# Kernel optimization log

Hardware: AMD Instinct MI355X
Metric: run time of the kernel (lower is better)

## Reference

```python
import jax, jax.numpy as jnp
import numpy as np

B, N, IN = 4, 1024, 768
H, F = 8, 96
ALPHA = 0.2
NEG = -1e30  # stands in for -inf in masked_fill; exp underflows to 0 identically


def setup_inputs() -> dict:
    key = jax.random.key(0)
    k1, k2, k3, k4 = jax.random.split(key, 4)
    node_features = jax.random.normal(k1, (B, N, IN), dtype=jnp.float32)
    attention_mask = jax.random.randint(k2, (B, N), 0, 2, dtype=jnp.int32)
    # torch Linear(in, H*F, bias=False): y = x @ W  (W stored here as [in, H*F])
    W = jax.random.normal(k3, (IN, H * F), dtype=jnp.float32) * (1.0 / np.sqrt(IN))
    # torch Linear(2*F, 1, bias=False): a-vector of length 2*F, shared across heads
    a = jax.random.normal(k4, (2 * F,), dtype=jnp.float32) * (1.0 / np.sqrt(2 * F))
    return {"node_features": node_features, "attention_mask": attention_mask, "W": W, "a": a}


def reference(node_features, attention_mask, W, a):
    b, n, _ = node_features.shape
    Wh = (node_features @ W).reshape(b, n, H, F)          # [B,N,H,F]
    a1, a2 = a[:F], a[F:]                                  # split additive attention vector
    # a([Wh_i ; Wh_j]) = Wh_i.a1 + Wh_j.a2  -> broadcast-add, no (B,N,N,H,2F) concat
    f1 = jnp.einsum('bnhf,f->bhn', Wh, a1)                 # query half [B,H,N]
    f2 = jnp.einsum('bnhf,f->bhn', Wh, a2)                 # key half   [B,H,N]
    e = f1[:, :, :, None] + f2[:, :, None, :]              # [B,H,N,N] (i=query, j=key)
    e = jnp.where(e >= 0, e, ALPHA * e)                    # leaky_relu
    mask = (attention_mask == 0)[:, None, None, :]         # mask keys j
    e = jnp.where(mask, NEG, e)
    attn = jax.nn.softmax(e, axis=-1)                      # [B,H,N,N]
    h = jnp.einsum('bhij,bjhf->bihf', attn, Wh)            # [B,N,H,F]
    return h.reshape(b, n, H * F)                          # concat=True
```

## Files before the change

kernel.cpp:

```cpp
#include <hip/hip_runtime.h>
#include <hip/hip_bf16.h>

#define ALPHA 0.2f
#define LOG2E 1.44269504f

#define VB_OFFB 0
#define XB_OFFB 6291456
#define WB_OFFB (XB_OFFB + 6291456)
#define F1P_OFFB (WB_OFFB + 1179648)
#define F2P_OFFB (F1P_OFFB + 786432)

typedef __attribute__((ext_vector_type(8))) unsigned short us8;
typedef __attribute__((ext_vector_type(8))) short s8;
typedef __attribute__((ext_vector_type(4))) float f32x4;
typedef __attribute__((ext_vector_type(4))) unsigned int u32x4;

__device__ inline unsigned short f2bf(float x) {
    __hip_bfloat16 h = __float2bfloat16(x);
    return reinterpret_cast<unsigned short&>(h);
}

__device__ __forceinline__ void gload16(const void* g, void* lds) {
    __builtin_amdgcn_global_load_lds((const unsigned int*)g, (unsigned int*)lds,
                                     16, 0, 0);
}

__global__ __launch_bounds__(256) void prep_all(const float* __restrict__ X,
                                                const float* __restrict__ W,
                                                unsigned short* __restrict__ Xb,
                                                unsigned short* __restrict__ Wb) {
    if (blockIdx.x < 1536) {
        const int i = (blockIdx.x * 256 + threadIdx.x) * 8;
        float4 v0 = *(const float4*)&X[i];
        float4 v1 = *(const float4*)&X[i + 4];
        ushort4 p0, p1;
        p0.x = f2bf(v0.x); p0.y = f2bf(v0.y); p0.z = f2bf(v0.z); p0.w = f2bf(v0.w);
        p1.x = f2bf(v1.x); p1.y = f2bf(v1.y); p1.z = f2bf(v1.z); p1.w = f2bf(v1.w);
        *(ushort4*)&Xb[i] = p0;
        *(ushort4*)&Xb[i + 4] = p1;
    } else {
        const int id = (blockIdx.x - 1536) * 256 + threadIdx.x;
        const int l = id & 63;
        const int ks = (id >> 6) & 1;
        const int cg4 = (id >> 7) & 3;
        const int kc = id >> 9;
        const int kt = kc / 12;
        const int ct = kc - kt * 12;
        const int k0 = kt * 64 + ks * 32 + (l >> 4) * 8;
        const int n = ct * 64 + cg4 * 16 + (l & 15);
        ushort4 p0, p1;
        p0.x = f2bf(W[(size_t)(k0 + 0) * 768 + n]);
        p0.y = f2bf(W[(size_t)(k0 + 1) * 768 + n]);
        p0.z = f2bf(W[(size_t)(k0 + 2) * 768 + n]);
        p0.w = f2bf(W[(size_t)(k0 + 3) * 768 + n]);
        p1.x = f2bf(W[(size_t)(k0 + 4) * 768 + n]);
        p1.y = f2bf(W[(size_t)(k0 + 5) * 768 + n]);
        p1.z = f2bf(W[(size_t)(k0 + 6) * 768 + n]);
        p1.w = f2bf(W[(size_t)(k0 + 7) * 768 + n]);
        *(ushort4*)&Wb[(size_t)id * 8 + 0] = p0;
        *(ushort4*)&Wb[(size_t)id * 8 + 4] = p1;
    }
}

__global__ __launch_bounds__(256) void gemm_s(const unsigned short* __restrict__ Xb,
                                              const unsigned short* __restrict__ Wb,
                                              const float* __restrict__ a,
                                              unsigned short* __restrict__ Vb,
                                              float* __restrict__ f1p,
                                              float* __restrict__ f2p) {
    __shared__ __align__(16) unsigned short Xs[2][4096];
    __shared__ __align__(16) unsigned short Ws[2][4096];

    const int tid = threadIdx.x;
    const int l = tid & 63;
    const int w = tid >> 6;
    const int wr = w >> 1, wc = w & 1;
    const int nid = (blockIdx.x & 7) * 96 + (blockIdx.x >> 3);
    const int bx = nid % 12;
    const int row0 = (nid / 12) * 64;

    const int xrow_base = w * 16 + (l >> 3);
    const int xkb_log8 = ((l & 7) ^ (l >> 3)) * 8;

    f32x4 acc[2][2];
#pragma unroll
    for (int i = 0; i < 2; ++i)
#pragma unroll
        for (int j = 0; j < 2; ++j) acc[i][j] = (f32x4){0.f, 0.f, 0.f, 0.f};

#pragma unroll
    for (int q = 0; q < 2; ++q) {
        const int g16 = w * 2 + q;
        gload16(Xb + (size_t)(row0 + xrow_base + q * 8) * 768 + xkb_log8,
                &Xs[0][g16 * 512]);
        gload16(Wb + (size_t)(0 * 12 + bx) * 4096 + g16 * 512 + l * 8,
                &Ws[0][g16 * 512]);
    }

    int buf = 0;
    for (int kt = 0; kt < 12; ++kt) {
        __syncthreads();
        if (kt < 11) {
            const int k0n = (kt + 1) * 64;
#pragma unroll
            for (int q = 0; q < 2; ++q) {
                const int g16 = w * 2 + q;
                gload16(Xb + (size_t)(row0 + xrow_base + q * 8) * 768 + k0n + xkb_log8,
                        &Xs[buf ^ 1][g16 * 512]);
                gload16(Wb + (size_t)((kt + 1) * 12 + bx) * 4096 + g16 * 512 + l * 8,
                        &Ws[buf ^ 1][g16 * 512]);
            }
        }
#pragma unroll
        for (int ks = 0; ks < 2; ++ks) {
            s8 af[2], bfr[2];
#pragma unroll
            for (int fr = 0; fr < 2; ++fr) {
                const int row = wr * 32 + fr * 16 + (l & 15);
                const int slot = (ks * 4 + (l >> 4)) ^ (row & 7);
                af[fr] = *(const s8*)((const char*)&Xs[buf][0] + row * 128 + slot * 16);
            }
#pragma unroll
            for (int cg = 0; cg < 2; ++cg) {
                bfr[cg] = *(const s8*)((const char*)&Ws[buf][0] +
                                       (((wc * 2 + cg) * 2 + ks) * 64 + l) * 16);
            }
#pragma unroll
            for (int fr = 0; fr < 2; ++fr)
#pragma unroll
                for (int cg = 0; cg < 2; ++cg)
                    acc[fr][cg] = __builtin_amdgcn_mfma_f32_16x16x32_bf16(
                        af[fr], bfr[cg], acc[fr][cg], 0, 0, 0);
        }
        buf ^= 1;
    }

#pragma unroll
    for (int fr = 0; fr < 2; ++fr) {
#pragma unroll
        for (int cg = 0; cg < 2; ++cg) {
            const int jglob = row0 + wr * 32 + fr * 16 + (l >> 4) * 4;
            const int b = jglob >> 10;
            const int jn = jglob & 1023;
            const int jc = jn >> 7;
            const int ks4 = (jn >> 5) & 3;
            const int kg = (jn >> 3) & 3;
            const int e0 = jn & 7;
            const int g0 = bx * 64 + wc * 32 + cg * 16;
            const int h = g0 / 96;
            const int ft = (g0 - h * 96) >> 4;
            const int fc = l & 15;
            const size_t ibase =
                (((((size_t)(b * 8 + h) * 8 + jc) * 4 + ks4) * 4 + kg) * 6 + ft) * 128 +
                fc * 8 + e0;
            ushort4 pk;
            pk.x = f2bf(acc[fr][cg][0]);
            pk.y = f2bf(acc[fr][cg][1]);
            pk.z = f2bf(acc[fr][cg][2]);
            pk.w = f2bf(acc[fr][cg][3]);
            *(ushort4*)&Vb[ibase] = pk;
        }
    }

#pragma unroll
    for (int cg = 0; cg < 2; ++cg) {
        const int c = bx * 64 + wc * 32 + cg * 16 + (l & 15);
        const int h = c / 96;
        const int f = c - h * 96;
        const float av1 = a[f];
        const float av2 = a[96 + f];
        const int g = bx * 4 + wc * 2 + cg;
#pragma unroll
        for (int fr = 0; fr < 2; ++fr) {
            const int jglob = row0 + wr * 32 + fr * 16 + (l >> 4) * 4;
#pragma unroll
            for (int r = 0; r < 4; ++r) {
                float s1 = acc[fr][cg][r] * av1;
                float s2 = acc[fr][cg][r] * av2;
#pragma unroll
                for (int m = 1; m < 16; m <<= 1) {
                    s1 += __shfl_xor(s1, m);
                    s2 += __shfl_xor(s2, m);
                }
                if ((l & 15) == 0) {
                    f1p[(size_t)(jglob + r) * 48 + g] = s1;
                    f2p[(size_t)(jglob + r) * 48 + g] = s2;
                }
            }
        }
    }
}

__global__ __launch_bounds__(256) void attn_fast(const unsigned short* __restrict__ Vb,
                                                 const float* __restrict__ f1p,
                                                 const float* __restrict__ f2p,
                                                 const int* __restrict__ mask,
                                                 float* __restrict__ out) {
    __shared__ __align__(16) unsigned short Vs[2][12288];
    __shared__ float g2_s[1024];

    const int tid = threadIdx.x;
    const int lane = tid & 63;
    const int w = tid >> 6;
    const int kg = lane >> 4;
    const int fcr = lane & 15;
    const int nid = (blockIdx.x & 7) * 64 + (blockIdx.x >> 3);
    const int it = nid & 15;
    const int bh = nid >> 4;
    const int b = bh >> 3;
    const int h = bh & 7;

    const size_t vbase = (size_t)bh * 98304;

    for (int j = tid; j < 1024; j += 256) {
        const float* p2 = f2p + (size_t)(b * 1024 + j) * 48 + h * 6;
        float s = ((p2[0] + p2[1]) + (p2[2] + p2[3])) + (p2[4] + p2[5]);
        g2_s[j] = (mask[b * 1024 + j] != 0) ? s * LOG2E : -20000.f;
    }
    const float* p1 = f1p + (size_t)(b * 1024 + it * 64 + w * 16 + fcr) * 48 + h * 6;
    const float f1v = (((p1[0] + p1[1]) + (p1[2] + p1[3])) + (p1[4] + p1[5])) * LOG2E;

#pragma unroll
    for (int r = 0; r < 6; ++r) {
        const int s = r * 256 + tid;
        gload16(Vb + vbase + (size_t)s * 8, &Vs[0][s * 8]);
    }

    f32x4 acc[6];
#pragma unroll
    for (int ft = 0; ft < 6; ++ft) acc[ft] = (f32x4){0.f, 0.f, 0.f, 0.f};
    float ls = 0.f;

    int buf = 0;
    for (int c = 0; c < 8; ++c) {
        __syncthreads();
        if (c < 7) {
#pragma unroll
            for (int r = 0; r < 6; ++r) {
                const int s = r * 256 + tid;
                gload16(Vb + vbase + (size_t)(c + 1) * 12288 + (size_t)s * 8,
                        &Vs[buf ^ 1][s * 8]);
            }
        }
        const unsigned short* vsb = &Vs[buf][0];
#pragma unroll
        for (int ks = 0; ks < 4; ++ks) {
            const int jb = c * 128 + ks * 32 + kg * 8;
            float4 ga = *(const float4*)&g2_s[jb];
            float4 gb = *(const float4*)&g2_s[jb + 4];
            float g[8] = {ga.x, ga.y, ga.z, ga.w, gb.x, gb.y, gb.z, gb.w};
            u32x4 afu;
#pragma unroll
            for (int ep = 0; ep < 4; ++ep) {
                float t0 = f1v + g[2 * ep];
                float t1 = f1v + g[2 * ep + 1];
                float l0 = fmaxf(t0, ALPHA * t0);
                float l1 = fmaxf(t1, ALPHA * t1);
                float p0 = exp2f(l0);
                float p1 = exp2f(l1);
                ls += p0 + p1;
                unsigned int pk;
                asm("v_cvt_pk_bf16_f32 %0, %1, %2" : "=v"(pk) : "v"(p0), "v"(p1));
                afu[ep] = pk;
            }
            s8 af = __builtin_bit_cast(s8, afu);
            const unsigned short* vp = vsb + ((ks * 4 + kg) * 6) * 128 + fcr * 8;
#pragma unroll
            for (int ft = 0; ft < 6; ++ft) {
                us8 bvu = *(const us8*)(vp + ft * 128);
                acc[ft] = __builtin_amdgcn_mfma_f32_16x16x32_bf16(
                    af, (s8)bvu, acc[ft], 0, 0, 0);
            }
        }
        buf ^= 1;
    }

    ls += __shfl_xor(ls, 16);
    ls += __shfl_xor(ls, 32);
    float inv[4];
#pragma unroll
    for (int r = 0; r < 4; ++r) inv[r] = 1.0f / __shfl(ls, kg * 4 + r);

    const int irow0 = it * 64 + w * 16 + kg * 4;
#pragma unroll
    for (int r = 0; r < 4; ++r) {
        const size_t ob = (size_t)(b * 1024 + irow0 + r) * 768 + h * 96 + fcr;
#pragma unroll
        for (int ft = 0; ft < 6; ++ft) {
            out[ob + ft * 16] = acc[ft][r] * inv[r];
        }
    }
}

extern "C" void kernel_launch(void* const* d_in, const int* in_sizes, int n_in,
                              void* d_out, int out_size, void* d_ws, size_t ws_size,
                              hipStream_t stream) {
    const float* X = (const float*)d_in[0];
    const int* mask = (const int*)d_in[1];
    const float* W = (const float*)d_in[2];
    const float* a = (const float*)d_in[3];
    float* out = (float*)d_out;
    char* ws = (char*)d_ws;

    unsigned short* Vb = (unsigned short*)(ws + VB_OFFB);
    unsigned short* Xb = (unsigned short*)(ws + XB_OFFB);
    unsigned short* Wb = (unsigned short*)(ws + WB_OFFB);
    float* f1p = (float*)(ws + F1P_OFFB);
    float* f2p = (float*)(ws + F2P_OFFB);

    prep_all<<<1824, 256, 0, stream>>>(X, W, Xb, Wb);
    gemm_s<<<768, 256, 0, stream>>>(Xb, Wb, a, Vb, f1p, f2p);
    attn_fast<<<512, 256, 0, stream>>>(Vb, f1p, f2p, mask, out);
}
```

Baseline: 50.45 us.

## Pre-swizzle X into MFMA fragment layout and load GEMM operands directly to registers

The prep kernel now writes X in bf16 directly in the per-lane MFMA A-fragment order (16-row tiles by 32-k slots), matching the existing pre-packed W layout. The GEMM then drops LDS staging and barriers entirely, loading each wave's fragments straight from global memory into registers with a register double buffer. This removes LDS traffic and __syncthreads. In exchange, operands that were shared between waves in a block are now re-read from global/L2 by each wave, and the prep kernel's X reads become strided rather than contiguous.

```diff
diff --git a/kernel.cpp b/kernel.cpp
--- a/kernel.cpp
+++ b/kernel.cpp
@@ -5,8 +5,8 @@
 #define LOG2E 1.44269504f
 
 #define VB_OFFB 0
-#define XB_OFFB 6291456
-#define WB_OFFB (XB_OFFB + 6291456)
+#define XF_OFFB 6291456
+#define WB_OFFB (XF_OFFB + 6291456)
 #define F1P_OFFB (WB_OFFB + 1179648)
 #define F2P_OFFB (F1P_OFFB + 786432)
 
@@ -27,17 +27,24 @@
 
 __global__ __launch_bounds__(256) void prep_all(const float* __restrict__ X,
                                                 const float* __restrict__ W,
-                                                unsigned short* __restrict__ Xb,
+                                                unsigned short* __restrict__ Xf,
                                                 unsigned short* __restrict__ Wb) {
     if (blockIdx.x < 1536) {
-        const int i = (blockIdx.x * 256 + threadIdx.x) * 8;
-        float4 v0 = *(const float4*)&X[i];
-        float4 v1 = *(const float4*)&X[i + 4];
+        const int f = blockIdx.x * 256 + threadIdx.x;
+        const int l = f & 63;
+        const int t = f >> 6;
+        const int kslot = t % 24;
+        const int rt = t / 24;
+        const int row = rt * 16 + (l & 15);
+        const int k0 = kslot * 32 + (l >> 4) * 8;
+        const float* xp = X + (size_t)row * 768 + k0;
+        float4 v0 = *(const float4*)xp;
+        float4 v1 = *(const float4*)(xp + 4);
         ushort4 p0, p1;
         p0.x = f2bf(v0.x); p0.y = f2bf(v0.y); p0.z = f2bf(v0.z); p0.w = f2bf(v0.w);
         p1.x = f2bf(v1.x); p1.y = f2bf(v1.y); p1.z = f2bf(v1.z); p1.w = f2bf(v1.w);
-        *(ushort4*)&Xb[i] = p0;
-        *(ushort4*)&Xb[i + 4] = p1;
+        *(ushort4*)&Xf[(size_t)f * 8 + 0] = p0;
+        *(ushort4*)&Xf[(size_t)f * 8 + 4] = p1;
     } else {
         const int id = (blockIdx.x - 1536) * 256 + threadIdx.x;
         const int l = id & 63;
@@ -62,15 +69,12 @@
     }
 }
 
-__global__ __launch_bounds__(256) void gemm_s(const unsigned short* __restrict__ Xb,
-                                              const unsigned short* __restrict__ Wb,
+__global__ __launch_bounds__(256) void gemm_r(const unsigned short* __restrict__ Xf_,
+                                              const unsigned short* __restrict__ Wb_,
                                               const float* __restrict__ a,
                                               unsigned short* __restrict__ Vb,
                                               float* __restrict__ f1p,
                                               float* __restrict__ f2p) {
-    __shared__ __align__(16) unsigned short Xs[2][4096];
-    __shared__ __align__(16) unsigned short Ws[2][4096];
-
     const int tid = threadIdx.x;
     const int l = tid & 63;
     const int w = tid >> 6;
@@ -78,9 +82,14 @@
     const int nid = (blockIdx.x & 7) * 96 + (blockIdx.x >> 3);
     const int bx = nid % 12;
     const int row0 = (nid / 12) * 64;
-
-    const int xrow_base = w * 16 + (l >> 3);
-    const int xkb_log8 = ((l & 7) ^ (l >> 3)) * 8;
+    const int rt0 = (nid / 12) * 4;
+
+    const us8* Xf = (const us8*)Xf_;
+    const us8* Wf = (const us8*)Wb_;
+
+    const us8* xb0 = Xf + ((size_t)(rt0 + wr * 2 + 0) * 24) * 64 + l;
+    const us8* xb1 = Xf + ((size_t)(rt0 + wr * 2 + 1) * 24) * 64 + l;
+    const us8* wb0 = Wf + (size_t)bx * 512 + (size_t)(wc * 2) * 128 + l;
 
     f32x4 acc[2][2];
 #pragma unroll
@@ -88,51 +97,39 @@
 #pragma unroll
         for (int j = 0; j < 2; ++j) acc[i][j] = (f32x4){0.f, 0.f, 0.f, 0.f};
 
-#pragma unroll
-    for (int q = 0; q < 2; ++q) {
-        const int g16 = w * 2 + q;
-        gload16(Xb + (size_t)(row0 + xrow_base + q * 8) * 768 + xkb_log8,
-                &Xs[0][g16 * 512]);
-        gload16(Wb + (size_t)(0 * 12 + bx) * 4096 + g16 * 512 + l * 8,
-                &Ws[0][g16 * 512]);
-    }
-
-    int buf = 0;
+    s8 af[2][2][2];
+    s8 bf[2][2][2];
+
+#pragma unroll
+    for (int ks = 0; ks < 2; ++ks) {
+        af[0][0][ks] = (s8)xb0[ks * 64];
+        af[0][1][ks] = (s8)xb1[ks * 64];
+        bf[0][0][ks] = (s8)wb0[ks * 64];
+        bf[0][1][ks] = (s8)wb0[128 + ks * 64];
+    }
+
+#pragma unroll
     for (int kt = 0; kt < 12; ++kt) {
-        __syncthreads();
+        const int cur = kt & 1;
+        const int nxt = cur ^ 1;
         if (kt < 11) {
-            const int k0n = (kt + 1) * 64;
-#pragma unroll
-            for (int q = 0; q < 2; ++q) {
-                const int g16 = w * 2 + q;
-                gload16(Xb + (size_t)(row0 + xrow_base + q * 8) * 768 + k0n + xkb_log8,
-                        &Xs[buf ^ 1][g16 * 512]);
-                gload16(Wb + (size_t)((kt + 1) * 12 + bx) * 4096 + g16 * 512 + l * 8,
-                        &Ws[buf ^ 1][g16 * 512]);
-            }
-        }
-#pragma unroll
-        for (int ks = 0; ks < 2; ++ks) {
-            s8 af[2], bfr[2];
-#pragma unroll
-            for (int fr = 0; fr < 2; ++fr) {
-                const int row = wr * 32 + fr * 16 + (l & 15);
-                const int slot = (ks * 4 + (l >> 4)) ^ (row & 7);
-                af[fr] = *(const s8*)((const char*)&Xs[buf][0] + row * 128 + slot * 16);
-            }
-#pragma unroll
-            for (int cg = 0; cg < 2; ++cg) {
-                bfr[cg] = *(const s8*)((const char*)&Ws[buf][0] +
-                                       (((wc * 2 + cg) * 2 + ks) * 64 + l) * 16);
-            }
+            const int kn = kt + 1;
+#pragma unroll
+            for (int ks = 0; ks < 2; ++ks) {
+                af[nxt][0][ks] = (s8)xb0[(kn * 2 + ks) * 64];
+                af[nxt][1][ks] = (s8)xb1[(kn * 2 + ks) * 64];
+                bf[nxt][0][ks] = (s8)wb0[(size_t)kn * 6144 + ks * 64];
+                bf[nxt][1][ks] = (s8)wb0[(size_t)kn * 6144 + 128 + ks * 64];
+            }
+        }
+#pragma unroll
+        for (int ks = 0; ks < 2; ++ks)
 #pragma unroll
             for (int fr = 0; fr < 2; ++fr)
 #pragma unroll
                 for (int cg = 0; cg < 2; ++cg)
                     acc[fr][cg] = __builtin_amdgcn_mfma_f32_16x16x32_bf16(
-                        af[fr], bfr[cg], acc[fr][cg], 0, 0, 0);
-        }
-        buf ^= 1;
+                        af[cur][fr][ks], bf[cur][cg][ks], acc[fr][cg], 0, 0, 0);
     }
 
 #pragma unroll
@@ -303,12 +300,12 @@
     char* ws = (char*)d_ws;
 
     unsigned short* Vb = (unsigned short*)(ws + VB_OFFB);
-    unsigned short* Xb = (unsigned short*)(ws + XB_OFFB);
+    unsigned short* Xf = (unsigned short*)(ws + XF_OFFB);
     unsigned short* Wb = (unsigned short*)(ws + WB_OFFB);
     float* f1p = (float*)(ws + F1P_OFFB);
     float* f2p = (float*)(ws + F2P_OFFB);
 
-    prep_all<<<1824, 256, 0, stream>>>(X, W, Xb, Wb);
-    gemm_s<<<768, 256, 0, stream>>>(Xb, Wb, a, Vb, f1p, f2p);
+    prep_all<<<1824, 256, 0, stream>>>(X, W, Xf, Wb);
+    gemm_r<<<768, 256, 0, stream>>>(Xf, Wb, a, Vb, f1p, f2p);
     attn_fast<<<512, 256, 0, stream>>>(Vb, f1p, f2p, mask, out);
 }
```

Result: no change. 51.30 us (+1.7%).
